# Kernel tuning notes

Measured on AMD Instinct MI355X. Metric: run time of the kernel, lower is better.

## Reference

```python
import jax, jax.numpy as jnp
import numpy as np

SR = 48000          # sample_rate
N = 480000          # num_samples
MAX_DELAYS = 50     # max_num_delays


def one_pole_lowpass(x, a):
    # y[n] = a*x[n] + (1-a)*y[n-1], zero initial state (causal one-pole IIR)
    def step(y, xn):
        y = a * xn + (1.0 - a) * y
        return y, y
    _, ys = jax.lax.scan(step, jnp.zeros((), x.dtype), x)
    return ys


def one_pole_bandpass(x, low, high):
    # bandpass as difference of two one-pole lowpasses (high cutoff minus low cutoff)
    return one_pole_lowpass(x, high) - one_pole_lowpass(x, low)


def setup_inputs() -> dict:
    key = jax.random.key(0)
    k1, k2, k3 = jax.random.split(key, 3)
    input_signal = jax.random.normal(k1, (N,), dtype=jnp.float32)
    parameters = jax.random.uniform(k2, (5,), dtype=jnp.float32)
    delay_buffer = jax.random.normal(k3, (N,), dtype=jnp.float32)
    return {"input_signal": input_signal, "parameters": parameters, "delay_buffer": delay_buffer}


def reference(input_signal, parameters, delay_buffer):
    frequency = jnp.clip(parameters[0], 20.0, SR / 2)
    feedback = jnp.clip(parameters[1], 0.0, 0.99)
    filter_low = jnp.clip(parameters[2], 1e-7, 0.99)
    filter_high = jnp.clip(parameters[3], 1e-7, 0.99)
    gain = jnp.maximum(parameters[4], 1e-7)

    delay_length = jnp.clip(jnp.floor(SR / frequency), 1, N // 2).astype(jnp.int32)
    num_delays = jnp.minimum(N // delay_length, MAX_DELAYS)

    taps = jnp.arange(1, MAX_DELAYS, dtype=jnp.int32)          # i = 1..49
    shifts = taps * delay_length                                # delay_start per tap
    powers = feedback ** taps.astype(jnp.float32)               # feedback^i
    active = (taps < num_delays) & (shifts < N)                 # loop bounds / break mask

    # The one-pole bandpass is linear and causal, so filtering the truncated,
    # scaled segment equals scaling + truncating the filtered full buffer.
    filtered = one_pole_bandpass(delay_buffer, filter_low, filter_high)  # [N]

    rolled = jax.vmap(lambda s: jnp.roll(filtered, s))(shifts)  # [49, N]
    pos = jnp.arange(N)
    valid = (pos[None, :] >= shifts[:, None]) & active[:, None]
    contrib = jnp.where(valid, rolled * powers[:, None], 0.0)   # [49, N]

    output_signal = input_signal + contrib.sum(axis=0)
    return jnp.tanh(output_signal * gain)
```

## Files before the change

### kernel.cpp

```cpp
#include <hip/hip_runtime.h>
#include <math.h>

#define SRATE 48000
#define NN    480000
#define MAXD  50
#define TPB   256
#define NV4   (NN / 4)
#define NBLKS ((NV4 + TPB - 1) / TPB)
#define NTAPB (NN / TPB)

__device__ __forceinline__ float clampf(float v, float lo, float hi) {
    return fminf(fmaxf(v, lo), hi);
}

struct Params { float al, bl, ah, bh, feedback, gain; int dl, nd; };

__device__ __forceinline__ Params load_params(const float* __restrict__ p) {
    Params q;
    float freq  = clampf(p[0], 20.0f, (float)(SRATE / 2));
    q.feedback  = clampf(p[1], 0.0f, 0.99f);
    float alow  = clampf(p[2], 1e-7f, 0.99f);
    float ahigh = clampf(p[3], 1e-7f, 0.99f);
    q.gain      = fmaxf(p[4], 1e-7f);
    float dlf   = clampf(floorf((float)SRATE / freq), 1.0f, (float)(NN / 2));
    q.dl = (int)dlf;
    q.nd = min(NN / q.dl, MAXD);
    q.al = alow;  q.bl = 1.0f - alow;
    q.ah = ahigh; q.bh = 1.0f - ahigh;
    return q;
}

__device__ __forceinline__ void seg_affine(const float4& v, float a, float b,
                                           float& Y, float& D) {
    float t = v.x;
    t = fmaf(t, b, v.y);
    t = fmaf(t, b, v.z);
    t = fmaf(t, b, v.w);
    Y = a * t;
    float b2 = b * b;
    D = b2 * b2;
}

__device__ __forceinline__ void wave_scan(int lane, float& Yl, float& Dl,
                                          float& Yh, float& Dh) {
    for (int off = 1; off < 64; off <<= 1) {
        float pYl = __shfl_up(Yl, off), pDl = __shfl_up(Dl, off);
        float pYh = __shfl_up(Yh, off), pDh = __shfl_up(Dh, off);
        if (lane >= off) {
            Yl = fmaf(Dl, pYl, Yl); Dl *= pDl;
            Yh = fmaf(Dh, pYh, Yh); Dh *= pDh;
        }
    }
}

__global__ __launch_bounds__(TPB) void scan_agg(
    const float* __restrict__ x, const float* __restrict__ p,
    float4* __restrict__ blkAgg)
{
    Params q = load_params(p);
    int tid = threadIdx.x;
    int t = blockIdx.x * TPB + tid;
    float Yl = 0.f, Dl = 1.f, Yh = 0.f, Dh = 1.f;
    if (t < NV4) {
        float4 v = ((const float4*)x)[t];
        seg_affine(v, q.al, q.bl, Yl, Dl);
        seg_affine(v, q.ah, q.bh, Yh, Dh);
    }
    int lane = tid & 63;
    wave_scan(lane, Yl, Dl, Yh, Dh);

    __shared__ float wYl[4], wDl[4], wYh[4], wDh[4];
    int w = tid >> 6;
    if (lane == 63) { wYl[w] = Yl; wDl[w] = Dl; wYh[w] = Yh; wDh[w] = Dh; }
    __syncthreads();
    if (tid == TPB - 1) {
        float cYl = 0.f, cDl = 1.f, cYh = 0.f, cDh = 1.f;
        for (int j = 0; j < 3; ++j) {
            cYl = fmaf(wDl[j], cYl, wYl[j]); cDl *= wDl[j];
            cYh = fmaf(wDh[j], cYh, wYh[j]); cDh *= wDh[j];
        }
        float AYl = fmaf(Dl, cYl, Yl), ADl = Dl * cDl;
        float AYh = fmaf(Dh, cYh, Yh), ADh = Dh * cDh;
        blkAgg[blockIdx.x] = make_float4(AYl, ADl, AYh, ADh);
    }
}

__global__ __launch_bounds__(TPB) void scan_apply(
    const float* __restrict__ x, const float* __restrict__ p,
    const float4* __restrict__ blkAgg,
    float* __restrict__ filtered)
{
    Params q = load_params(p);
    int tid = threadIdx.x;
    int lane = tid & 63;
    int w = tid >> 6;
    int t = blockIdx.x * TPB + tid;
    bool valid = (t < NV4);

    float4 v = make_float4(0.f, 0.f, 0.f, 0.f);
    float Yl = 0.f, Dl = 1.f, Yh = 0.f, Dh = 1.f;
    if (valid) {
        v = ((const float4*)x)[t];
        seg_affine(v, q.al, q.bl, Yl, Dl);
        seg_affine(v, q.ah, q.bh, Yh, Dh);
    }
    wave_scan(lane, Yl, Dl, Yh, Dh);

    __shared__ float wYl[4], wDl[4], wYh[4], wDh[4];
    if (lane == 63) { wYl[w] = Yl; wDl[w] = Dl; wYh[w] = Yh; wDh[w] = Dh; }

    __shared__ float sYl[TPB], sDl[TPB], sYh[TPB], sDh[TPB];
    {
        int i2 = 2 * tid;
        float4 a0 = (i2     < NBLKS) ? blkAgg[i2]     : make_float4(0.f, 1.f, 0.f, 1.f);
        float4 a1 = (i2 + 1 < NBLKS) ? blkAgg[i2 + 1] : make_float4(0.f, 1.f, 0.f, 1.f);
        sYl[tid] = fmaf(a1.y, a0.x, a1.x); sDl[tid] = a1.y * a0.y;
        sYh[tid] = fmaf(a1.w, a0.z, a1.z); sDh[tid] = a1.w * a0.w;
    }
    __syncthreads();
    for (int off = 1; off < TPB; off <<= 1) {
        float cyl = sYl[tid], cdl = sDl[tid], cyh = sYh[tid], cdh = sDh[tid];
        float pyl = 0.f, pdl = 1.f, pyh = 0.f, pdh = 1.f;
        bool has = (tid >= off);
        if (has) { pyl = sYl[tid-off]; pdl = sDl[tid-off];
                   pyh = sYh[tid-off]; pdh = sDh[tid-off]; }
        __syncthreads();
        if (has) {
            sYl[tid] = fmaf(cdl, pyl, cyl); sDl[tid] = cdl * pdl;
            sYh[tid] = fmaf(cdh, pyh, cyh); sDh[tid] = cdh * pdh;
        }
        __syncthreads();
    }
    __shared__ float GYl_s, GYh_s;
    if (tid == 0) {
        int b = blockIdx.x;
        int qq = b >> 1;
        float GYl = 0.f, GDl = 1.f, GYh = 0.f, GDh = 1.f;
        if (qq > 0) { GYl = sYl[qq-1]; GDl = sDl[qq-1];
                      GYh = sYh[qq-1]; GDh = sDh[qq-1]; }
        if (b & 1) {
            float4 am = blkAgg[2 * qq];
            GYl = fmaf(am.y, GYl, am.x); GDl = am.y * GDl;
            GYh = fmaf(am.w, GYh, am.z); GDh = am.w * GDh;
        }
        (void)GDl; (void)GDh;
        GYl_s = GYl; GYh_s = GYh;
    }
    __syncthreads();

    float eYl = __shfl_up(Yl, 1), eDl = __shfl_up(Dl, 1);
    float eYh = __shfl_up(Yh, 1), eDh = __shfl_up(Dh, 1);
    if (lane == 0) { eYl = 0.f; eDl = 1.f; eYh = 0.f; eDh = 1.f; }
    float cYl = 0.f, cDl = 1.f, cYh = 0.f, cDh = 1.f;
    for (int j = 0; j < 3; ++j) {
        if (j < w) {
            cYl = fmaf(wDl[j], cYl, wYl[j]); cDl *= wDl[j];
            cYh = fmaf(wDh[j], cYh, wYh[j]); cDh *= wDh[j];
        }
    }
    float BYl = fmaf(eDl, cYl, eYl), BDl = eDl * cDl;
    float BYh = fmaf(eDh, cYh, eYh), BDh = eDh * cDh;
    float yl = fmaf(BDl, GYl_s, BYl);
    float yh = fmaf(BDh, GYh_s, BYh);

    if (valid) {
        float4 o;
        yl = fmaf(q.bl, yl, q.al * v.x); yh = fmaf(q.bh, yh, q.ah * v.x); o.x = yh - yl;
        yl = fmaf(q.bl, yl, q.al * v.y); yh = fmaf(q.bh, yh, q.ah * v.y); o.y = yh - yl;
        yl = fmaf(q.bl, yl, q.al * v.z); yh = fmaf(q.bh, yh, q.ah * v.z); o.z = yh - yl;
        yl = fmaf(q.bl, yl, q.al * v.w); yh = fmaf(q.bh, yh, q.ah * v.w); o.w = yh - yl;
        ((float4*)filtered)[t] = o;
    }
}

__global__ __launch_bounds__(TPB) void taps_kernel(
    const float* __restrict__ input, const float* __restrict__ p,
    const float* __restrict__ filtered, float* __restrict__ out)
{
    int n = blockIdx.x * TPB + threadIdx.x;
    if (n >= NN) return;
    Params q = load_params(p);
    float acc = input[n];
    int m = min(q.nd - 1, n / q.dl);
    int s = q.dl;
    float w = q.feedback;
    for (int i = 1; i <= m; ++i) {
        acc = fmaf(w, filtered[n - s], acc);
        s += q.dl;
        w *= q.feedback;
    }
    out[n] = tanhf(acc * q.gain);
}

extern "C" void kernel_launch(void* const* d_in, const int* in_sizes, int n_in,
                              void* d_out, int out_size, void* d_ws, size_t ws_size,
                              hipStream_t stream)
{
    const float* input  = (const float*)d_in[0];
    const float* params = (const float*)d_in[1];
    const float* dbuf   = (const float*)d_in[2];
    float* out = (float*)d_out;

    float* ws       = (float*)d_ws;
    float* filtered = ws;
    float4* blkAgg  = (float4*)(ws + NN);

    scan_agg  <<<NBLKS, TPB, 0, stream>>>(dbuf, params, blkAgg);
    scan_apply<<<NBLKS, TPB, 0, stream>>>(dbuf, params, blkAgg, filtered);
    taps_kernel<<<NTAPB, TPB, 0, stream>>>(input, params, filtered, out);
}
```

Before: 76.70 us.

## Fuse scan and tap kernels into one cooperative kernel with grid syncs

Merges the three launches (block aggregate scan, scan apply, tap accumulation) into a single cooperative kernel that uses grid.sync between phases. The filtered data is no longer recomputed from scratch in a second launch; the register state from phase one is reused. The tap phase now handles four outputs per thread with strided indices and iterates over all taps using predicated loads instead of a per-thread trip count. This removes launch gaps and duplicate loads but adds grid-wide barrier cost and requires all 469 blocks to be co-resident.

```diff
diff --git a/kernel.cpp b/kernel.cpp
--- a/kernel.cpp
+++ b/kernel.cpp
@@ -1,13 +1,16 @@
 #include <hip/hip_runtime.h>
+#include <hip/hip_cooperative_groups.h>
 #include <math.h>
+
+namespace cg = cooperative_groups;
 
 #define SRATE 48000
 #define NN    480000
 #define MAXD  50
 #define TPB   256
 #define NV4   (NN / 4)
-#define NBLKS ((NV4 + TPB - 1) / TPB)
-#define NTAPB (NN / TPB)
+#define GBLK  ((NV4 + TPB - 1) / TPB)
+#define GTHR  (GBLK * TPB)
 
 __device__ __forceinline__ float clampf(float v, float lo, float hi) {
     return fminf(fmaxf(v, lo), hi);
@@ -53,25 +56,30 @@
     }
 }
 
-__global__ __launch_bounds__(TPB) void scan_agg(
-    const float* __restrict__ x, const float* __restrict__ p,
-    float4* __restrict__ blkAgg)
+__global__ __launch_bounds__(TPB) void resonator_fused(
+    const float* __restrict__ input, const float* __restrict__ p,
+    const float* __restrict__ x, float* __restrict__ filtered,
+    float4* __restrict__ blkAgg, float* __restrict__ out)
 {
+    cg::grid_group grid = cg::this_grid();
     Params q = load_params(p);
-    int tid = threadIdx.x;
-    int t = blockIdx.x * TPB + tid;
+    const int tid  = threadIdx.x;
+    const int lane = tid & 63;
+    const int wv   = tid >> 6;
+    const int t    = blockIdx.x * TPB + tid;
+    const bool valid = (t < NV4);
+
+    float4 v = make_float4(0.f, 0.f, 0.f, 0.f);
     float Yl = 0.f, Dl = 1.f, Yh = 0.f, Dh = 1.f;
-    if (t < NV4) {
-        float4 v = ((const float4*)x)[t];
+    if (valid) {
+        v = ((const float4*)x)[t];
         seg_affine(v, q.al, q.bl, Yl, Dl);
         seg_affine(v, q.ah, q.bh, Yh, Dh);
     }
-    int lane = tid & 63;
     wave_scan(lane, Yl, Dl, Yh, Dh);
 
     __shared__ float wYl[4], wDl[4], wYh[4], wDh[4];
-    int w = tid >> 6;
-    if (lane == 63) { wYl[w] = Yl; wDl[w] = Dl; wYh[w] = Yh; wDh[w] = Dh; }
+    if (lane == 63) { wYl[wv] = Yl; wDl[wv] = Dl; wYh[wv] = Yh; wDh[wv] = Dh; }
     __syncthreads();
     if (tid == TPB - 1) {
         float cYl = 0.f, cDl = 1.f, cYh = 0.f, cDh = 1.f;
@@ -83,37 +91,14 @@
         float AYh = fmaf(Dh, cYh, Yh), ADh = Dh * cDh;
         blkAgg[blockIdx.x] = make_float4(AYl, ADl, AYh, ADh);
     }
-}
-
-__global__ __launch_bounds__(TPB) void scan_apply(
-    const float* __restrict__ x, const float* __restrict__ p,
-    const float4* __restrict__ blkAgg,
-    float* __restrict__ filtered)
-{
-    Params q = load_params(p);
-    int tid = threadIdx.x;
-    int lane = tid & 63;
-    int w = tid >> 6;
-    int t = blockIdx.x * TPB + tid;
-    bool valid = (t < NV4);
-
-    float4 v = make_float4(0.f, 0.f, 0.f, 0.f);
-    float Yl = 0.f, Dl = 1.f, Yh = 0.f, Dh = 1.f;
-    if (valid) {
-        v = ((const float4*)x)[t];
-        seg_affine(v, q.al, q.bl, Yl, Dl);
-        seg_affine(v, q.ah, q.bh, Yh, Dh);
-    }
-    wave_scan(lane, Yl, Dl, Yh, Dh);
-
-    __shared__ float wYl[4], wDl[4], wYh[4], wDh[4];
-    if (lane == 63) { wYl[w] = Yl; wDl[w] = Dl; wYh[w] = Yh; wDh[w] = Dh; }
+    __threadfence();
+    grid.sync();
 
     __shared__ float sYl[TPB], sDl[TPB], sYh[TPB], sDh[TPB];
     {
         int i2 = 2 * tid;
-        float4 a0 = (i2     < NBLKS) ? blkAgg[i2]     : make_float4(0.f, 1.f, 0.f, 1.f);
-        float4 a1 = (i2 + 1 < NBLKS) ? blkAgg[i2 + 1] : make_float4(0.f, 1.f, 0.f, 1.f);
+        float4 a0 = (i2     < GBLK) ? blkAgg[i2]     : make_float4(0.f, 1.f, 0.f, 1.f);
+        float4 a1 = (i2 + 1 < GBLK) ? blkAgg[i2 + 1] : make_float4(0.f, 1.f, 0.f, 1.f);
         sYl[tid] = fmaf(a1.y, a0.x, a1.x); sDl[tid] = a1.y * a0.y;
         sYh[tid] = fmaf(a1.w, a0.z, a1.z); sDh[tid] = a1.w * a0.w;
     }
@@ -153,7 +138,7 @@
     if (lane == 0) { eYl = 0.f; eDl = 1.f; eYh = 0.f; eDh = 1.f; }
     float cYl = 0.f, cDl = 1.f, cYh = 0.f, cDh = 1.f;
     for (int j = 0; j < 3; ++j) {
-        if (j < w) {
+        if (j < wv) {
             cYl = fmaf(wDl[j], cYl, wYl[j]); cDl *= wDl[j];
             cYh = fmaf(wDh[j], cYh, wYh[j]); cDh *= wDh[j];
         }
@@ -171,25 +156,37 @@
         yl = fmaf(q.bl, yl, q.al * v.w); yh = fmaf(q.bh, yh, q.ah * v.w); o.w = yh - yl;
         ((float4*)filtered)[t] = o;
     }
-}
-
-__global__ __launch_bounds__(TPB) void taps_kernel(
-    const float* __restrict__ input, const float* __restrict__ p,
-    const float* __restrict__ filtered, float* __restrict__ out)
-{
-    int n = blockIdx.x * TPB + threadIdx.x;
-    if (n >= NN) return;
-    Params q = load_params(p);
-    float acc = input[n];
-    int m = min(q.nd - 1, n / q.dl);
+    __threadfence();
+    grid.sync();
+
+    const int g  = blockIdx.x * TPB + tid;
+    const int n0 = g;
+    const int n1 = g + GTHR;
+    const int n2 = g + 2 * GTHR;
+    const int n3 = g + 3 * GTHR;
+    float acc0 = input[n0];
+    float acc1 = input[n1];
+    float acc2 = input[n2];
+    float acc3 = (n3 < NN) ? input[n3] : 0.f;
     int s = q.dl;
-    float w = q.feedback;
-    for (int i = 1; i <= m; ++i) {
-        acc = fmaf(w, filtered[n - s], acc);
+    float wgt = q.feedback;
+    for (int i = 1; i < q.nd; ++i) {
+        int a0 = n0 - s, a1 = n1 - s, a2 = n2 - s, a3 = n3 - s;
+        float f0 = (a0 >= 0) ? filtered[a0] : 0.f;
+        float f1 = (a1 >= 0) ? filtered[a1] : 0.f;
+        float f2 = (a2 >= 0) ? filtered[a2] : 0.f;
+        float f3 = (a3 >= 0 && n3 < NN) ? filtered[a3] : 0.f;
+        acc0 = fmaf(wgt, f0, acc0);
+        acc1 = fmaf(wgt, f1, acc1);
+        acc2 = fmaf(wgt, f2, acc2);
+        acc3 = fmaf(wgt, f3, acc3);
         s += q.dl;
-        w *= q.feedback;
-    }
-    out[n] = tanhf(acc * q.gain);
+        wgt *= q.feedback;
+    }
+    out[n0] = tanhf(acc0 * q.gain);
+    out[n1] = tanhf(acc1 * q.gain);
+    out[n2] = tanhf(acc2 * q.gain);
+    if (n3 < NN) out[n3] = tanhf(acc3 * q.gain);
 }
 
 extern "C" void kernel_launch(void* const* d_in, const int* in_sizes, int n_in,
@@ -205,7 +202,8 @@
     float* filtered = ws;
     float4* blkAgg  = (float4*)(ws + NN);
 
-    scan_agg  <<<NBLKS, TPB, 0, stream>>>(dbuf, params, blkAgg);
-    scan_apply<<<NBLKS, TPB, 0, stream>>>(dbuf, params, blkAgg, filtered);
-    taps_kernel<<<NTAPB, TPB, 0, stream>>>(input, params, filtered, out);
-}
+    void* args[] = { (void*)&input, (void*)&params, (void*)&dbuf,
+                     (void*)&filtered, (void*)&blkAgg, (void*)&out };
+    (void)hipLaunchCooperativeKernel((void*)resonator_fused, dim3(GBLK), dim3(TPB),
+                                     args, 0, stream);
+}
```

New measurement: 242.6 us. 3.16x slower.
